# Kernel optimization log

Measured on AMD Instinct MI355X. Metric: run time of the kernel, lower is better.

Reference implementation:

```python
import jax, jax.numpy as jnp
import numpy as np

B, S, D, H = 4, 1024, 1024, 16
DH = D // H  # head dim = 64
PAD = -1e7   # padding_num in source
EPS = 1e-3   # keras LayerNormalization default epsilon


def setup_inputs() -> dict:
    key = jax.random.key(0)
    ks = jax.random.split(key, 8)
    return {
        "queries": jax.random.normal(ks[0], (B, S, D), jnp.float32),
        "keys": jax.random.normal(ks[1], (B, S, D), jnp.float32),
        "values": jax.random.normal(ks[2], (B, S, D), jnp.float32),
        "query_masks": jax.random.randint(ks[3], (B, S), 0, 2, jnp.int32),
        "key_masks": jax.random.randint(ks[4], (B, S), 0, 2, jnp.int32),
        "Wq": jax.random.normal(ks[5], (D, D), jnp.float32) * (D ** -0.5),
        "Wk": jax.random.normal(ks[6], (D, D), jnp.float32) * (D ** -0.5),
        "Wv": jax.random.normal(ks[7], (D, D), jnp.float32) * (D ** -0.5),
        "gamma": jnp.ones((D,), jnp.float32),
        "beta": jnp.zeros((D,), jnp.float32),
    }


def reference(queries, keys, values, query_masks, key_masks, Wq, Wk, Wv, gamma, beta):
    # QKV projections (no bias)
    Q = queries @ Wq  # [B,S,D]
    K = keys @ Wk
    V = values @ Wv
    # split heads: tf.split(axis=2)+concat(axis=0) == head-major layout [H,B,S,DH]
    Qh = Q.reshape(B, S, H, DH).transpose(2, 0, 1, 3)
    Kh = K.reshape(B, S, H, DH).transpose(2, 0, 1, 3)
    Vh = V.reshape(B, S, H, DH).transpose(2, 0, 1, 3)
    # scaled scores; note source scales by head_dim ** 0.5 (d_k of split K)
    scores = jnp.einsum("hbqd,hbkd->hbqk", Qh, Kh) / (DH ** 0.5)
    # additive key mask: positions where key_mask==0 get large negative
    scores = jnp.where(key_masks[None, :, None, :] == 0, PAD, scores)
    attn = jax.nn.softmax(scores, axis=-1)
    # multiplicative query mask AFTER softmax (as in source)
    attn = attn * query_masks[None, :, :, None].astype(jnp.float32)
    out = jnp.einsum("hbqk,hbkd->hbqd", attn, Vh)  # [H,B,S,DH]
    # merge heads back: concat over feature axis in head order
    out = out.transpose(1, 2, 0, 3).reshape(B, S, D)
    # residual + LayerNorm
    res = queries + out
    mean = jnp.mean(res, axis=-1, keepdims=True)
    var = jnp.mean(jnp.square(res - mean), axis=-1, keepdims=True)
    return gamma * (res - mean) * jax.lax.rsqrt(var + EPS) + beta
```

## Files before the change

### kernel.cpp

```cpp
#include <hip/hip_runtime.h>

#define BB   4
#define SS   1024
#define DD   1024
#define HH   16
#define DHH  64
#define LN_EPS  (1e-3f)

typedef unsigned short u16;
typedef __attribute__((ext_vector_type(8))) short bf16x8;
typedef __attribute__((ext_vector_type(4))) float f32x4;

__device__ __forceinline__ u16 f2bf(float f) {
    union { float f; unsigned int u; } v; v.f = f;
    return (u16)((v.u + 0x7FFFu + ((v.u >> 16) & 1u)) >> 16);
}

__device__ __forceinline__ void cp16(void* lds, const void* g) {
    __builtin_amdgcn_global_load_lds(
        (const __attribute__((address_space(1))) unsigned int*)g,
        (__attribute__((address_space(3))) unsigned int*)lds, 16, 0, 0);
}

__global__ __launch_bounds__(256) void prep(const float* __restrict__ q,
                                            const float* __restrict__ k,
                                            const float* __restrict__ v,
                                            const float* __restrict__ Wq,
                                            const float* __restrict__ Wk,
                                            const float* __restrict__ Wv,
                                            u16* __restrict__ Abf,
                                            u16* __restrict__ WtA) {
    __shared__ float Ts[64][65];
    const int z = blockIdx.z;
    const int tid = threadIdx.x;
    if (z < 3) {
        const float* src = (z == 0) ? q : (z == 1) ? k : v;
        u16* dst = Abf + (size_t)z * ((size_t)BB * SS * DD);
        const int N8 = BB * SS * DD / 8;
        for (int i = blockIdx.x * 256 + tid; i < N8; i += 256 * 256) {
            const float4 f0 = ((const float4*)src)[i * 2];
            const float4 f1 = ((const float4*)src)[i * 2 + 1];
            union { u16 u[8]; uint4 o; } t;
            t.u[0] = f2bf(f0.x); t.u[1] = f2bf(f0.y);
            t.u[2] = f2bf(f0.z); t.u[3] = f2bf(f0.w);
            t.u[4] = f2bf(f1.x); t.u[5] = f2bf(f1.y);
            t.u[6] = f2bf(f1.z); t.u[7] = f2bf(f1.w);
            ((uint4*)dst)[i] = t.o;
        }
    } else {
        const float* W = (z == 3) ? Wq : (z == 4) ? Wk : Wv;
        u16* Wt = WtA + (size_t)(z - 3) * DD * DD;
        const int k0 = (blockIdx.x >> 4) * 64, n0 = (blockIdx.x & 15) * 64;
        #pragma unroll
        for (int it = 0; it < 4; ++it) {
            const int idx = tid + it * 256;
            const int r = idx >> 4, c4 = (idx & 15) * 4;
            const float4 vv = *(const float4*)&W[(size_t)(k0 + r) * DD + n0 + c4];
            Ts[r][c4 + 0] = vv.x; Ts[r][c4 + 1] = vv.y;
            Ts[r][c4 + 2] = vv.z; Ts[r][c4 + 3] = vv.w;
        }
        __syncthreads();
        const int n = tid >> 2, kc = (tid & 3) * 16;
        #pragma unroll
        for (int p = 0; p < 8; ++p) {
            const unsigned int lo = f2bf(Ts[kc + p * 2 + 0][n]);
            const unsigned int hi = f2bf(Ts[kc + p * 2 + 1][n]);
            *(unsigned int*)&Wt[(size_t)(n0 + n) * DD + k0 + kc + p * 2] = lo | (hi << 16);
        }
    }
}

__global__ __launch_bounds__(512, 2) void gemm_fused(const u16* __restrict__ Abf,
                                                     const u16* __restrict__ WtA,
                                                     u16* __restrict__ Qbf,
                                                     u16* __restrict__ Kbf,
                                                     u16* __restrict__ Vtb) {
    __shared__ u16 lds[2][2][2][8192];

    const int bid = blockIdx.x;
    const int swz = (bid & 7) * 24 + (bid >> 3);
    const int z   = swz >> 6;
    const int rem = swz & 63;
    const int m0  = (rem >> 2) * 256;
    const int n0  = (rem & 3) * 256;

    const u16* A  = Abf + (size_t)z * ((size_t)BB * SS * DD);
    const u16* Bm = WtA + (size_t)z * (DD * DD);

    const int tid  = threadIdx.x;
    const int wave = tid >> 6, lane = tid & 63;
    const int ln = lane & 15, quad = lane >> 4;
    const int wr = wave >> 2, wc = wave & 3;

    int r_[2], c_[2];
    #pragma unroll
    for (int rd = 0; rd < 2; ++rd) {
        const int l = rd * 512 + tid;
        const int rr = l >> 2, cs = l & 3;
        r_[rd] = rr;
        c_[rd] = cs ^ ((rr >> 1) & 3);
    }
    const u16* srcA[2] = { A  + (size_t)(m0 + r_[0]) * DD + c_[0] * 8,
                           A  + (size_t)(m0 + r_[1]) * DD + c_[1] * 8 };
    const u16* srcB[2] = { Bm + (size_t)(n0 + r_[0]) * DD + c_[0] * 8,
                           Bm + (size_t)(n0 + r_[1]) * DD + c_[1] * 8 };

    int offA[8], offB[4];
    #pragma unroll
    for (int mi = 0; mi < 8; ++mi) {
        const int r = wr * 128 + mi * 16 + ln;
        offA[mi] = (r * 4 + (quad ^ ((r >> 1) & 3))) * 8;
    }
    #pragma unroll
    for (int nj = 0; nj < 4; ++nj) {
        const int r = wc * 64 + nj * 16 + ln;
        offB[nj] = (r * 4 + (quad ^ ((r >> 1) & 3))) * 8;
    }

    auto stage = [&](int T, int x) {
        const int cb = T & 1;
        const int koff = T * 64 + x * 32;
        #pragma unroll
        for (int rd = 0; rd < 2; ++rd) {
            cp16(&lds[cb][x][0][(rd * 512 + wave * 64) * 8], srcA[rd] + koff);
            cp16(&lds[cb][x][1][(rd * 512 + wave * 64) * 8], srcB[rd] + koff);
        }
    };

    f32x4 acc[8][4] = {};

    stage(0, 0); stage(0, 1); stage(1, 0);
    asm volatile("s_waitcnt vmcnt(8)" ::: "memory");
    __builtin_amdgcn_s_barrier();

    #pragma unroll
    for (int t = 0; t < 16; ++t) {
        const int c = t & 1;
        #pragma unroll
        for (int x = 0; x < 2; ++x) {
            if (x == 0) { if (t < 15) stage(t + 1, 1); }
            else        { if (t < 14) stage(t + 2, 0); }

            bf16x8 af[8], bfv[4];
            const u16* Ar = &lds[c][x][0][0];
            const u16* Br = &lds[c][x][1][0];
            #pragma unroll
            for (int mi = 0; mi < 8; ++mi) af[mi] = *(const bf16x8*)&Ar[offA[mi]];
            #pragma unroll
            for (int nj = 0; nj < 4; ++nj) bfv[nj] = *(const bf16x8*)&Br[offB[nj]];

            if (x == 0) {
                if (t < 15) asm volatile("s_waitcnt vmcnt(8)" ::: "memory");
                else        asm volatile("s_waitcnt vmcnt(0)" ::: "memory");
            } else {
                if (t < 14)       asm volatile("s_waitcnt vmcnt(8)" ::: "memory");
                else if (t == 14) asm volatile("s_waitcnt vmcnt(4)" ::: "memory");
            }
            __builtin_amdgcn_s_barrier();

            __builtin_amdgcn_s_setprio(1);
            #pragma unroll
            for (int mi = 0; mi < 8; ++mi)
                #pragma unroll
                for (int nj = 0; nj < 4; ++nj)
                    acc[mi][nj] = __builtin_amdgcn_mfma_f32_16x16x32_bf16(
                        af[mi], bfv[nj], acc[mi][nj], 0, 0, 0);
            __builtin_amdgcn_s_setprio(0);
            __builtin_amdgcn_s_barrier();
        }
    }

    const int hh = (n0 >> 6) + wc;
    if (z < 2) {
        u16* C = (z == 0) ? Qbf : Kbf;
        const float scale = (z == 0) ? 0.125f : 1.0f;
        #pragma unroll
        for (int mi = 0; mi < 8; ++mi) {
            const int mbase = m0 + wr * 128 + mi * 16 + quad * 4;
            const int bb = mbase >> 10, sb = mbase & 1023;
            #pragma unroll
            for (int nj = 0; nj < 4; ++nj) {
                const int dh = nj * 16 + ln;
                #pragma unroll
                for (int r = 0; r < 4; ++r)
                    C[(((size_t)bb * HH + hh) * SS + sb + r) * DHH + dh] =
                        f2bf(acc[mi][nj][r] * scale);
            }
        }
    } else {
        #pragma unroll
        for (int mi = 0; mi < 8; ++mi) {
            const int mbase = m0 + wr * 128 + mi * 16 + quad * 4;
            const int bb = mbase >> 10, sb = mbase & 1023;
            #pragma unroll
            for (int nj = 0; nj < 4; ++nj) {
                const int dh = nj * 16 + ln;
                uint2 pk;
                pk.x = (unsigned int)f2bf(acc[mi][nj][0]) | ((unsigned int)f2bf(acc[mi][nj][1]) << 16);
                pk.y = (unsigned int)f2bf(acc[mi][nj][2]) | ((unsigned int)f2bf(acc[mi][nj][3]) << 16);
                *(uint2*)&Vtb[(((size_t)bb * HH + hh) * DHH + dh) * SS + sb] = pk;
            }
        }
    }
}

__global__ __launch_bounds__(256) void attn_mfma(const u16* __restrict__ Qg,
                                                 const u16* __restrict__ Kg,
                                                 const u16* __restrict__ Vtg,
                                                 const int* __restrict__ qmask,
                                                 const int* __restrict__ kmask,
                                                 float* __restrict__ O) {
    __shared__ u16 QPs[64 * 68];
    __shared__ u16 Ks[64 * 64];
    __shared__ u16 Vs[64 * 64];

    const int bid  = blockIdx.x;
    const int xcd  = bid & 7;
    const int rest = bid >> 3;
    const int bh   = (rest & 7) * 8 + xcd;
    const int qt   = rest >> 3;
    const int b    = bh >> 4, h = bh & 15;
    const int q0   = qt * 64;
    const int tid  = threadIdx.x;
    const int wave = tid >> 6, lane = tid & 63;
    const int ln = lane & 15, quad = lane >> 4;
    const size_t bhs = (size_t)b * HH + h;

    #pragma unroll
    for (int w = 0; w < 2; ++w) {
        const int s = w * 256 + wave * 64 + lane;
        const int r = s >> 3, csrc = (s & 7) ^ (r & 7);
        cp16(&QPs[(size_t)(w * 256 + wave * 64) * 8],
             &Qg[(bhs * SS + q0 + r) * DHH + csrc * 8]);
    }
    __syncthreads();

    bf16x8 qf[2];
    #pragma unroll
    for (int kk = 0; kk < 2; ++kk) {
        const int r = wave * 16 + ln;
        qf[kk] = *(const bf16x8*)&QPs[((r << 3) + ((kk * 4 + quad) ^ (r & 7))) << 3];
    }

    f32x4 o[4] = {};
    float lsum[4] = {0.f, 0.f, 0.f, 0.f};
    const f32x4 zero = {0.f, 0.f, 0.f, 0.f};

    for (int kt = 0; kt < SS / 64; ++kt) {
        __syncthreads();
        #pragma unroll
        for (int w = 0; w < 2; ++w) {
            const int s = w * 256 + wave * 64 + lane;
            const int r = s >> 3, csrc = (s & 7) ^ (r & 7);
            cp16(&Ks[(size_t)(w * 256 + wave * 64) * 8],
                 &Kg[(bhs * SS + kt * 64 + r) * DHH + csrc * 8]);
            cp16(&Vs[(size_t)(w * 256 + wave * 64) * 8],
                 &Vtg[(bhs * DHH + r) * SS + kt * 64 + csrc * 8]);
        }
        __syncthreads();

        #pragma unroll
        for (int nt = 0; nt < 4; ++nt) {
            const int krow = nt * 16 + ln;
            const bf16x8 k0f = *(const bf16x8*)&Ks[((krow << 3) + ((0 + quad) ^ (krow & 7))) << 3];
            const bf16x8 k1f = *(const bf16x8*)&Ks[((krow << 3) + ((4 + quad) ^ (krow & 7))) << 3];
            f32x4 sacc = __builtin_amdgcn_mfma_f32_16x16x32_bf16(qf[0], k0f, zero, 0, 0, 0);
            sacc = __builtin_amdgcn_mfma_f32_16x16x32_bf16(qf[1], k1f, sacc, 0, 0, 0);
            const int km = kmask[b * SS + kt * 64 + krow];
            #pragma unroll
            for (int r = 0; r < 4; ++r) {
                const float p = km ? __expf(sacc[r]) : 0.0f;
                lsum[r] += p;
                QPs[(wave * 16 + quad * 4 + r) * 68 + nt * 16 + ln] = f2bf(p);
            }
        }

        #pragma unroll
        for (int kk2 = 0; kk2 < 2; ++kk2) {
            const bf16x8 pf = *(const bf16x8*)&QPs[(wave * 16 + ln) * 68 + kk2 * 32 + quad * 8];
            #pragma unroll
            for (int nt2 = 0; nt2 < 4; ++nt2) {
                const int vrow = nt2 * 16 + ln;
                const bf16x8 vf = *(const bf16x8*)&Vs[((vrow << 3) + ((kk2 * 4 + quad) ^ (vrow & 7))) << 3];
                o[nt2] = __builtin_amdgcn_mfma_f32_16x16x32_bf16(pf, vf, o[nt2], 0, 0, 0);
            }
        }
    }

    #pragma unroll
    for (int r = 0; r < 4; ++r) {
        #pragma unroll
        for (int off = 1; off < 16; off <<= 1)
            lsum[r] += __shfl_xor(lsum[r], off);
        const int q = q0 + wave * 16 + quad * 4 + r;
        const float scale = (float)qmask[b * SS + q] / lsum[r];
        #pragma unroll
        for (int nt2 = 0; nt2 < 4; ++nt2)
            O[((size_t)b * SS + q) * DD + h * DHH + nt2 * 16 + ln] = o[nt2][r] * scale;
    }
}

__global__ __launch_bounds__(256) void ln_kernel(const float* __restrict__ Qin,
                                                 const float* __restrict__ attn,
                                                 const float* __restrict__ gamma,
                                                 const float* __restrict__ beta,
                                                 float* __restrict__ out) {
    const int row = blockIdx.x;
    const int tid = threadIdx.x;
    const int wid = tid >> 6, lane = tid & 63;
    __shared__ float sred[4];

    const float4 qv = ((const float4*)Qin)[(size_t)row * 256 + tid];
    const float4 av = ((const float4*)attn)[(size_t)row * 256 + tid];
    float4 v;
    v.x = qv.x + av.x; v.y = qv.y + av.y;
    v.z = qv.z + av.z; v.w = qv.w + av.w;

    float sum = v.x + v.y + v.z + v.w;
    #pragma unroll
    for (int off = 32; off; off >>= 1) sum += __shfl_down(sum, off);
    if (lane == 0) sred[wid] = sum;
    __syncthreads();
    const float mean = (sred[0] + sred[1] + sred[2] + sred[3]) * (1.0f / DD);
    __syncthreads();

    const float dx = v.x - mean, dy = v.y - mean, dz = v.z - mean, dw = v.w - mean;
    float vs = dx * dx + dy * dy + dz * dz + dw * dw;
    #pragma unroll
    for (int off = 32; off; off >>= 1) vs += __shfl_down(vs, off);
    if (lane == 0) sred[wid] = vs;
    __syncthreads();
    const float var = (sred[0] + sred[1] + sred[2] + sred[3]) * (1.0f / DD);
    const float inv = rsqrtf(var + LN_EPS);

    const float4 g = ((const float4*)gamma)[tid];
    const float4 bt = ((const float4*)beta)[tid];
    float4 ov;
    ov.x = g.x * dx * inv + bt.x; ov.y = g.y * dy * inv + bt.y;
    ov.z = g.z * dz * inv + bt.z; ov.w = g.w * dw * inv + bt.w;
    ((float4*)out)[(size_t)row * 256 + tid] = ov;
}

extern "C" void kernel_launch(void* const* d_in, const int* in_sizes, int n_in,
                              void* d_out, int out_size, void* d_ws, size_t ws_size,
                              hipStream_t stream) {
    const float* queries = (const float*)d_in[0];
    const float* keys    = (const float*)d_in[1];
    const float* values  = (const float*)d_in[2];
    const int*   qmask   = (const int*)d_in[3];
    const int*   kmask   = (const int*)d_in[4];
    const float* Wq      = (const float*)d_in[5];
    const float* Wk      = (const float*)d_in[6];
    const float* Wv      = (const float*)d_in[7];
    const float* gamma   = (const float*)d_in[8];
    const float* beta    = (const float*)d_in[9];
    float* out = (float*)d_out;

    const size_t NTOK = (size_t)BB * SS;
    u16* Abf = (u16*)d_ws;
    float* Ob = (float*)d_ws;
    u16* Qbf = Abf + 3 * NTOK * DD;
    u16* Kbf = Qbf + NTOK * DD;
    u16* Vtb = Kbf + NTOK * DD;
    u16* WtA = Vtb + NTOK * DD;

    prep<<<dim3(256, 1, 6), 256, 0, stream>>>(queries, keys, values, Wq, Wk, Wv, Abf, WtA);

    gemm_fused<<<192, 512, 0, stream>>>(Abf, WtA, Qbf, Kbf, Vtb);

    attn_mfma<<<BB * HH * (SS / 64), 256, 0, stream>>>(Qbf, Kbf, Vtb, qmask, kmask, Ob);

    ln_kernel<<<BB * SS, 256, 0, stream>>>(queries, Ob, gamma, beta, out);
}
```

Measured before the change: 199.2 us.

## Double-buffer K/V tiles in attention and stage key mask in LDS

The attention kernel now double-buffers K and V tiles in LDS, prefetching tile kt+2 while computing on the current one and using explicit vmcnt waits instead of two full syncthreads per iteration. The key mask is converted once to floats in LDS and applied as a multiply. Q fragments are loaded directly from global memory. Scores are computed transposed so each lane holds one query row, which lets the row sum be done with fewer shuffles. The log2(e) factor is folded into the Q scale so exp2 can be used, and bf16 packing uses the hardware pack-convert instruction. This adds LDS usage and relies on hand-written wait counts being correct.

```diff
diff --git a/kernel.cpp b/kernel.cpp
--- a/kernel.cpp
+++ b/kernel.cpp
@@ -14,6 +14,12 @@
 __device__ __forceinline__ u16 f2bf(float f) {
     union { float f; unsigned int u; } v; v.f = f;
     return (u16)((v.u + 0x7FFFu + ((v.u >> 16) & 1u)) >> 16);
+}
+
+__device__ __forceinline__ unsigned int cvt_pk_bf16(float lo, float hi) {
+    unsigned int r;
+    asm("v_cvt_pk_bf16_f32 %0, %1, %2" : "=v"(r) : "v"(lo), "v"(hi));
+    return r;
 }
 
 __device__ __forceinline__ void cp16(void* lds, const void* g) {
@@ -173,7 +179,7 @@
     const int hh = (n0 >> 6) + wc;
     if (z < 2) {
         u16* C = (z == 0) ? Qbf : Kbf;
-        const float scale = (z == 0) ? 0.125f : 1.0f;
+        const float scale = (z == 0) ? 0.18033688f : 1.0f;
         #pragma unroll
         for (int mi = 0; mi < 8; ++mi) {
             const int mbase = m0 + wr * 128 + mi * 16 + quad * 4;
@@ -196,8 +202,8 @@
             for (int nj = 0; nj < 4; ++nj) {
                 const int dh = nj * 16 + ln;
                 uint2 pk;
-                pk.x = (unsigned int)f2bf(acc[mi][nj][0]) | ((unsigned int)f2bf(acc[mi][nj][1]) << 16);
-                pk.y = (unsigned int)f2bf(acc[mi][nj][2]) | ((unsigned int)f2bf(acc[mi][nj][3]) << 16);
+                pk.x = cvt_pk_bf16(acc[mi][nj][0], acc[mi][nj][1]);
+                pk.y = cvt_pk_bf16(acc[mi][nj][2], acc[mi][nj][3]);
                 *(uint2*)&Vtb[(((size_t)bb * HH + hh) * DHH + dh) * SS + sb] = pk;
             }
         }
@@ -210,9 +216,10 @@
                                                  const int* __restrict__ qmask,
                                                  const int* __restrict__ kmask,
                                                  float* __restrict__ O) {
-    __shared__ u16 QPs[64 * 68];
-    __shared__ u16 Ks[64 * 64];
-    __shared__ u16 Vs[64 * 64];
+    __shared__ u16 Ps[64 * 68];
+    __shared__ u16 Ks[2][64 * 64];
+    __shared__ u16 Vs[2][64 * 64];
+    __shared__ float kmLds[SS];
 
     const int bid  = blockIdx.x;
     const int xcd  = bid & 7;
@@ -226,74 +233,99 @@
     const int ln = lane & 15, quad = lane >> 4;
     const size_t bhs = (size_t)b * HH + h;
 
-    #pragma unroll
-    for (int w = 0; w < 2; ++w) {
-        const int s = w * 256 + wave * 64 + lane;
-        const int r = s >> 3, csrc = (s & 7) ^ (r & 7);
-        cp16(&QPs[(size_t)(w * 256 + wave * 64) * 8],
-             &Qg[(bhs * SS + q0 + r) * DHH + csrc * 8]);
-    }
-    __syncthreads();
-
-    bf16x8 qf[2];
-    #pragma unroll
-    for (int kk = 0; kk < 2; ++kk) {
-        const int r = wave * 16 + ln;
-        qf[kk] = *(const bf16x8*)&QPs[((r << 3) + ((kk * 4 + quad) ^ (r & 7))) << 3];
-    }
-
-    f32x4 o[4] = {};
-    float lsum[4] = {0.f, 0.f, 0.f, 0.f};
-    const f32x4 zero = {0.f, 0.f, 0.f, 0.f};
-
-    for (int kt = 0; kt < SS / 64; ++kt) {
-        __syncthreads();
+    auto stageKV = [&](int t) {
+        const int cb = t & 1;
         #pragma unroll
         for (int w = 0; w < 2; ++w) {
             const int s = w * 256 + wave * 64 + lane;
             const int r = s >> 3, csrc = (s & 7) ^ (r & 7);
-            cp16(&Ks[(size_t)(w * 256 + wave * 64) * 8],
-                 &Kg[(bhs * SS + kt * 64 + r) * DHH + csrc * 8]);
-            cp16(&Vs[(size_t)(w * 256 + wave * 64) * 8],
-                 &Vtg[(bhs * DHH + r) * SS + kt * 64 + csrc * 8]);
-        }
-        __syncthreads();
+            cp16(&Ks[cb][(w * 256 + wave * 64) * 8],
+                 &Kg[(bhs * SS + t * 64 + r) * DHH + csrc * 8]);
+            cp16(&Vs[cb][(w * 256 + wave * 64) * 8],
+                 &Vtg[(bhs * DHH + r) * SS + t * 64 + csrc * 8]);
+        }
+    };
+
+    const u16* qrow = &Qg[(bhs * SS + q0 + wave * 16 + ln) * DHH];
+    const bf16x8 qf0 = *(const bf16x8*)&qrow[quad * 8];
+    const bf16x8 qf1 = *(const bf16x8*)&qrow[32 + quad * 8];
+    asm volatile("" ::: "memory");
+    cp16(&kmLds[wave * 256], &kmask[b * SS + (wave * 64 + lane) * 4]);
+    stageKV(0);
+    stageKV(1);
+    asm volatile("s_waitcnt vmcnt(4)" ::: "memory");
+    __builtin_amdgcn_s_barrier();
+
+    {
+        const int4 iv = *(const int4*)&kmLds[tid * 4];
+        float4 fv;
+        fv.x = (float)iv.x; fv.y = (float)iv.y;
+        fv.z = (float)iv.z; fv.w = (float)iv.w;
+        *(float4*)&kmLds[tid * 4] = fv;
+    }
+    asm volatile("s_waitcnt lgkmcnt(0)" ::: "memory");
+    __builtin_amdgcn_s_barrier();
+
+    f32x4 o[4] = {};
+    float lsum = 0.f;
+    const f32x4 zero = {0.f, 0.f, 0.f, 0.f};
+    const int prow = (wave * 16 + ln) * 68;
+
+    #pragma unroll 2
+    for (int kt = 0; kt < SS / 64; ++kt) {
+        const int cb = kt & 1;
+        const u16* Kc = Ks[cb];
+        const u16* Vc = Vs[cb];
 
         #pragma unroll
         for (int nt = 0; nt < 4; ++nt) {
             const int krow = nt * 16 + ln;
-            const bf16x8 k0f = *(const bf16x8*)&Ks[((krow << 3) + ((0 + quad) ^ (krow & 7))) << 3];
-            const bf16x8 k1f = *(const bf16x8*)&Ks[((krow << 3) + ((4 + quad) ^ (krow & 7))) << 3];
-            f32x4 sacc = __builtin_amdgcn_mfma_f32_16x16x32_bf16(qf[0], k0f, zero, 0, 0, 0);
-            sacc = __builtin_amdgcn_mfma_f32_16x16x32_bf16(qf[1], k1f, sacc, 0, 0, 0);
-            const int km = kmask[b * SS + kt * 64 + krow];
-            #pragma unroll
-            for (int r = 0; r < 4; ++r) {
-                const float p = km ? __expf(sacc[r]) : 0.0f;
-                lsum[r] += p;
-                QPs[(wave * 16 + quad * 4 + r) * 68 + nt * 16 + ln] = f2bf(p);
-            }
+            const bf16x8 k0f = *(const bf16x8*)&Kc[((krow << 3) + ((0 + quad) ^ (krow & 7))) << 3];
+            const bf16x8 k1f = *(const bf16x8*)&Kc[((krow << 3) + ((4 + quad) ^ (krow & 7))) << 3];
+            f32x4 sacc = __builtin_amdgcn_mfma_f32_16x16x32_bf16(k0f, qf0, zero, 0, 0, 0);
+            sacc = __builtin_amdgcn_mfma_f32_16x16x32_bf16(k1f, qf1, sacc, 0, 0, 0);
+            const float4 fm = *(const float4*)&kmLds[kt * 64 + nt * 16 + quad * 4];
+            const float p0 = fm.x * __builtin_amdgcn_exp2f(sacc[0]);
+            const float p1 = fm.y * __builtin_amdgcn_exp2f(sacc[1]);
+            const float p2 = fm.z * __builtin_amdgcn_exp2f(sacc[2]);
+            const float p3 = fm.w * __builtin_amdgcn_exp2f(sacc[3]);
+            lsum += (p0 + p1) + (p2 + p3);
+            uint2 pk;
+            pk.x = cvt_pk_bf16(p0, p1);
+            pk.y = cvt_pk_bf16(p2, p3);
+            *(uint2*)&Ps[prow + nt * 16 + quad * 4] = pk;
         }
 
         #pragma unroll
         for (int kk2 = 0; kk2 < 2; ++kk2) {
-            const bf16x8 pf = *(const bf16x8*)&QPs[(wave * 16 + ln) * 68 + kk2 * 32 + quad * 8];
+            const bf16x8 pf = *(const bf16x8*)&Ps[prow + kk2 * 32 + quad * 8];
             #pragma unroll
             for (int nt2 = 0; nt2 < 4; ++nt2) {
                 const int vrow = nt2 * 16 + ln;
-                const bf16x8 vf = *(const bf16x8*)&Vs[((vrow << 3) + ((kk2 * 4 + quad) ^ (vrow & 7))) << 3];
+                const bf16x8 vf = *(const bf16x8*)&Vc[((vrow << 3) + ((kk2 * 4 + quad) ^ (vrow & 7))) << 3];
                 o[nt2] = __builtin_amdgcn_mfma_f32_16x16x32_bf16(pf, vf, o[nt2], 0, 0, 0);
             }
         }
-    }
-
+
+        if (kt == SS / 64 - 1) break;
+        __builtin_amdgcn_s_barrier();
+        if (kt + 2 < SS / 64) {
+            stageKV(kt + 2);
+            asm volatile("s_waitcnt vmcnt(4)" ::: "memory");
+        } else {
+            asm volatile("s_waitcnt vmcnt(0)" ::: "memory");
+        }
+        __builtin_amdgcn_s_barrier();
+    }
+
+    lsum += __shfl_xor(lsum, 16);
+    lsum += __shfl_xor(lsum, 32);
     #pragma unroll
     for (int r = 0; r < 4; ++r) {
-        #pragma unroll
-        for (int off = 1; off < 16; off <<= 1)
-            lsum[r] += __shfl_xor(lsum[r], off);
-        const int q = q0 + wave * 16 + quad * 4 + r;
-        const float scale = (float)qmask[b * SS + q] / lsum[r];
+        const int qloc = quad * 4 + r;
+        const float l = __shfl(lsum, qloc);
+        const int q = q0 + wave * 16 + qloc;
+        const float scale = (float)qmask[b * SS + q] / l;
         #pragma unroll
         for (int nt2 = 0; nt2 < 4; ++nt2)
             O[((size_t)b * SS + q) * DD + h * DHH + nt2 * 16 + ln] = o[nt2][r] * scale;
```

New measurement: 199.0 us. About the same (-0.1%).
